# Performance work log

Hardware: AMD Instinct MI355X
Metric: run time of the kernel (lower is better)

The kernel has to match this reference:

```python
import jax, jax.numpy as jnp
import numpy as np
import math

B, N, F = 32, 1024, 64      # batch, nodes, input_dim (data_size)
PRE = 64                     # preweight (== input_dim so output Linear works)
L1 = 128                     # layer_1


def setup_inputs() -> dict:
    key = jax.random.key(0)
    ks = jax.random.split(key, 12)
    def lin(k, out_d, in_d):
        bound = 1.0 / math.sqrt(in_d)
        kw, kb = jax.random.split(k)
        W = jax.random.uniform(kw, (out_d, in_d), jnp.float32, -bound, bound)
        b = jax.random.uniform(kb, (out_d,), jnp.float32, -bound, bound)
        return W, b
    W_pre, b_pre = lin(ks[0], PRE, F)
    W_fc1, b_fc1 = lin(ks[1], L1, PRE)
    W_keys, b_keys = lin(ks[2], 1, L1)
    W_out, b_out = lin(ks[3], 1, F)
    alpha = jax.random.uniform(ks[4], (1,), jnp.float32)
    x = jax.random.normal(ks[5], (B, N, F), jnp.float32)
    adjacency_matrix = jax.random.uniform(ks[6], (B, N, N), jnp.float32)
    return {
        "x": x, "adjacency_matrix": adjacency_matrix, "alpha": alpha,
        "W_pre": W_pre, "b_pre": b_pre, "W_fc1": W_fc1, "b_fc1": b_fc1,
        "W_keys": W_keys, "b_keys": b_keys, "W_out": W_out, "b_out": b_out,
    }


def reference(x, adjacency_matrix, alpha, W_pre, b_pre, W_fc1, b_fc1,
              W_keys, b_keys, W_out, b_out):
    # --- D^-1/2 A D^-1/2 normalization (D is diagonal -> row/col scaling) ---
    deg = adjacency_matrix.sum(axis=-1)                       # [B, N]
    deg = jnp.where(deg != 0, deg, 1.0)
    d_isqrt = deg ** -0.5                                     # [B, N]
    A_norm = d_isqrt[:, :, None] * adjacency_matrix * d_isqrt[:, None, :]
    # --- (alpha*I + A_norm) @ x ---
    h = alpha[0] * x + jnp.einsum('bij,bjf->bif', A_norm, x)  # [B, N, F]
    # --- node embedding (pre_weighting + relu) ---
    values = jax.nn.relu(h @ W_pre.T + b_pre)                 # [B, N, PRE]
    # --- attention pooling (dropout is identity at eval) ---
    queries = jax.nn.relu(values @ W_fc1.T + b_fc1)           # [B, N, L1]
    logits = (queries @ W_keys.T + b_keys)[..., 0]            # [B, N]
    scores = jax.nn.softmax(logits / math.sqrt(2.0), axis=-1) # [B, N]
    vect = jnp.einsum('bn,bnp->bp', scores, values)           # [B, PRE]
    y = vect @ W_out.T + b_out                                # [B, 1]
    return y
```

## Files before the change

kernel.cpp:

```cpp
#include <hip/hip_runtime.h>


#define N_ 1024
#define F_ 64

typedef short s16x8 __attribute__((ext_vector_type(8)));
typedef float f32x4 __attribute__((ext_vector_type(4)));
typedef unsigned short u16x8 __attribute__((ext_vector_type(8)));

__device__ __forceinline__ unsigned short bf16rne(float f) {
  union { float f; unsigned u; } v; v.f = f;
  unsigned r = v.u + 0x7fffu + ((v.u >> 16) & 1u);
  return (unsigned short)(r >> 16);
}

__device__ __forceinline__ void fma_row(float (&a)[4], const float4 av,
                                        const float4 x0, const float4 x1,
                                        const float4 x2, const float4 x3) {
  a[0] += av.x * x0.x + av.y * x1.x + av.z * x2.x + av.w * x3.x;
  a[1] += av.x * x0.y + av.y * x1.y + av.z * x2.y + av.w * x3.y;
  a[2] += av.x * x0.z + av.y * x1.z + av.z * x2.z + av.w * x3.z;
  a[3] += av.x * x0.w + av.y * x1.w + av.z * x2.w + av.w * x3.w;
}

__device__ __forceinline__ void stage16(const void* g, void* l) {
  auto gp = reinterpret_cast<const __attribute__((address_space(1))) void*>(
      reinterpret_cast<uintptr_t>(g));
  auto lp = reinterpret_cast<__attribute__((address_space(3))) void*>(
      reinterpret_cast<uintptr_t>(l));
  __builtin_amdgcn_global_load_lds(gp, lp, 16, 0, 0);
}

__global__ __launch_bounds__(256) void k_deg(const float* __restrict__ A,
                                             float* __restrict__ disq) {
  const int row  = blockIdx.x * 4 + (threadIdx.x >> 6);
  const int lane = threadIdx.x & 63;
  const float4* a4 = (const float4*)(A + (size_t)row * N_);
  float s = 0.f;
#pragma unroll
  for (int it = 0; it < 4; ++it) {
    float4 v = a4[it * 64 + lane];
    s += v.x + v.y + v.z + v.w;
  }
#pragma unroll
  for (int off = 32; off > 0; off >>= 1) s += __shfl_down(s, off, 64);
  if (lane == 0) {
    float d = (s != 0.f) ? s : 1.f;
    disq[row] = rsqrtf(d);
  }
}

__global__ __launch_bounds__(256) void k_xt(const float* __restrict__ x,
                                            const float* __restrict__ disq,
                                            unsigned short* __restrict__ xtb) {
  __shared__ float xs[64][68];
  const int b = blockIdx.y, j0 = blockIdx.x * 64, t = threadIdx.x;
  const float* xb = x + ((size_t)b << 16);
  const float* dq = disq + (b << 10);
#pragma unroll
  for (int it = 0; it < 4; ++it) {
    int idx = it * 1024 + t * 4;
    int jj = idx >> 6, ff = idx & 63;
    float4 vv = *(const float4*)&xb[(size_t)(j0 + jj) * F_ + ff];
    float sc = dq[j0 + jj];
    vv.x *= sc; vv.y *= sc; vv.z *= sc; vv.w *= sc;
    *(float4*)&xs[jj][ff] = vv;
  }
  __syncthreads();
  const int f = t & 63, ch = t >> 6;
  u16x8 o0, o1;
#pragma unroll
  for (int jj = 0; jj < 8; ++jj) o0[jj] = bf16rne(xs[ch * 16 + jj][f]);
#pragma unroll
  for (int jj = 0; jj < 8; ++jj) o1[jj] = bf16rne(xs[ch * 16 + 8 + jj][f]);
  unsigned short* dst = xtb + (size_t)(b * 64 + f) * N_ + j0 + ch * 16;
  *(u16x8*)dst = o0;
  *(u16x8*)(dst + 8) = o1;
}

__global__ __launch_bounds__(256, 3) void k_spmm_mlp(const float* __restrict__ Af,
                                                     const unsigned short* __restrict__ xtb,
                                                     const float* __restrict__ x,
                                                     const float* __restrict__ disq,
                                                     const float* __restrict__ alphap,
                                                     const float* __restrict__ Wpre,
                                                     const float* __restrict__ bpre,
                                                     const float* __restrict__ Wfc1,
                                                     const float* __restrict__ bfc1,
                                                     const float* __restrict__ Wkeys,
                                                     const float* __restrict__ bkeysp,
                                                     float* __restrict__ values,
                                                     float* __restrict__ logits) {
  __shared__ __attribute__((aligned(16))) char smem[54272];
  float (*hs)[68]   = (float(*)[68])(smem);
  float (*wft)[128] = (float(*)[128])(smem + 17408);
  float (*part)[16] = (float(*)[16])(smem + 50176);

  const int t  = threadIdx.x;
  const int b  = blockIdx.x;
  const int i0 = blockIdx.y * 64;
  const int w  = t >> 6, l = t & 63;
  const int lr = l & 15, kq = l >> 4;
  const size_t bb = ((size_t)b << 20);

  const int half = (w & 1) * 32;
  const int srow4 = l >> 4;
  const int mslot = l & 15;
  const float* gA0 = Af + bb + (size_t)(i0 + half + srow4) * 1024;
  int xoff[4];
#pragma unroll
  for (int q = 0; q < 4; ++q) xoff[q] = (mslot ^ ((q * 4 + srow4) & 15)) << 2;
  const int srow8 = l >> 3;
  const int schB  = ((l & 7) ^ srow8) * 8;
  const unsigned short* gsB = xtb + (size_t)(b * 64 + half + srow8) * N_ + schB;

  auto STAGE = [&](char* bufp, int ksv) {
    if (w < 2) {
      const int ko = ksv * 64;
#pragma unroll
      for (int j = 0; j < 8; ++j)
        stage16(gA0 + (size_t)j * 4096 + xoff[j & 3] + ko,
                bufp + (half + j * 4) * 256);
    } else {
      const int ko = ksv * 64;
#pragma unroll
      for (int j = 0; j < 4; ++j)
        stage16(gsB + (size_t)j * 8 * N_ + ko,
                bufp + 16384 + half * 128 + j * 1024);
    }
  };

  STAGE(smem, 0);
  __syncthreads();

  f32x4 acc0 = {0.f, 0.f, 0.f, 0.f}, acc1 = acc0, acc2 = acc0, acc3 = acc0;
  const int arow = w * 16 + lr;
  const int swB = (lr & 7) << 4;
  int cur = 0;

  for (int ks = 0; ks < 16; ++ks) {
    if (ks < 15) STAGE(smem + (cur ^ 1) * 24576, ks + 1);
    const char* cb = smem + cur * 24576;
#pragma unroll
    for (int s = 0; s < 2; ++s) {
      const int m0 = s * 8 + kq * 2;
      f32x4 alo = *(const f32x4*)(cb + arow * 256 + ((m0 ^ lr) << 4));
      f32x4 ahi = *(const f32x4*)(cb + arow * 256 + (((m0 + 1) ^ lr) << 4));
      s16x8 af;
      af[0] = (short)bf16rne(alo[0]); af[1] = (short)bf16rne(alo[1]);
      af[2] = (short)bf16rne(alo[2]); af[3] = (short)bf16rne(alo[3]);
      af[4] = (short)bf16rne(ahi[0]); af[5] = (short)bf16rne(ahi[1]);
      af[6] = (short)bf16rne(ahi[2]); af[7] = (short)bf16rne(ahi[3]);
      const int ch = ((kq + 4 * s) << 4);
      s16x8 b0 = *(const s16x8*)(cb + 16384 + (0 * 16 + lr) * 128 + (ch ^ swB));
      s16x8 b1 = *(const s16x8*)(cb + 16384 + (1 * 16 + lr) * 128 + (ch ^ swB));
      s16x8 b2 = *(const s16x8*)(cb + 16384 + (2 * 16 + lr) * 128 + (ch ^ swB));
      s16x8 b3 = *(const s16x8*)(cb + 16384 + (3 * 16 + lr) * 128 + (ch ^ swB));
      acc0 = __builtin_amdgcn_mfma_f32_16x16x32_bf16(af, b0, acc0, 0, 0, 0);
      acc1 = __builtin_amdgcn_mfma_f32_16x16x32_bf16(af, b1, acc1, 0, 0, 0);
      acc2 = __builtin_amdgcn_mfma_f32_16x16x32_bf16(af, b2, acc2, 0, 0, 0);
      acc3 = __builtin_amdgcn_mfma_f32_16x16x32_bf16(af, b3, acc3, 0, 0, 0);
    }
    __syncthreads();
    cur ^= 1;
  }

  const float alpha = alphap[0];
  const float* dq = disq + (b << 10);
  const float* xb = x + ((size_t)b << 16);
  const int rl = w * 16 + kq * 4;
#pragma unroll
  for (int r = 0; r < 4; ++r) {
    float di = dq[i0 + rl + r];
    size_t ro = (size_t)(i0 + rl + r) * F_;
    hs[rl + r][0  + lr] = alpha * xb[ro + 0  + lr] + di * acc0[r];
    hs[rl + r][16 + lr] = alpha * xb[ro + 16 + lr] + di * acc1[r];
    hs[rl + r][32 + lr] = alpha * xb[ro + 32 + lr] + di * acc2[r];
    hs[rl + r][48 + lr] = alpha * xb[ro + 48 + lr] + di * acc3[r];
  }
#pragma unroll
  for (int it = 0; it < 4; ++it) {
    int idx = it * 1024 + t * 4;
    float4 wv = *(const float4*)&Wpre[idx];
    int p = idx >> 6, f = idx & 63;
    wft[f + 0][p] = wv.x; wft[f + 1][p] = wv.y; wft[f + 2][p] = wv.z; wft[f + 3][p] = wv.w;
  }
  __syncthreads();

  const size_t base = ((size_t)(b * 16 + blockIdx.y)) * 4096;
  const int cg = t & 15, rg = t >> 4;
  float acc[4][4] = {{0.f}};
#pragma unroll
  for (int q = 0; q < 16; ++q) {
    float4 xv0 = *(float4*)&wft[q * 4 + 0][cg * 4];
    float4 xv1 = *(float4*)&wft[q * 4 + 1][cg * 4];
    float4 xv2 = *(float4*)&wft[q * 4 + 2][cg * 4];
    float4 xv3 = *(float4*)&wft[q * 4 + 3][cg * 4];
#pragma unroll
    for (int k = 0; k < 4; ++k) {
      float4 av = *(float4*)&hs[rg * 4 + k][q * 4];
      fma_row(acc[k], av, xv0, xv1, xv2, xv3);
    }
  }
  float4 bp = *(const float4*)&bpre[cg * 4];
  __syncthreads();
#pragma unroll
  for (int k = 0; k < 4; ++k) {
    float4 o;
    o.x = fmaxf(acc[k][0] + bp.x, 0.f);
    o.y = fmaxf(acc[k][1] + bp.y, 0.f);
    o.z = fmaxf(acc[k][2] + bp.z, 0.f);
    o.w = fmaxf(acc[k][3] + bp.w, 0.f);
    *(float4*)&hs[rg * 4 + k][cg * 4] = o;
    *(float4*)&values[base + (size_t)(rg * 4 + k) * 64 + cg * 4] = o;
  }
#pragma unroll
  for (int it = 0; it < 8; ++it) {
    int idx = it * 1024 + t * 4;
    int ll = idx >> 6, p = idx & 63;
    float4 wv = *(const float4*)&Wfc1[idx];
    wft[p + 0][ll] = wv.x; wft[p + 1][ll] = wv.y; wft[p + 2][ll] = wv.z; wft[p + 3][ll] = wv.w;
  }
  __syncthreads();

  const int lg = cg;
  float acc_a[4][4] = {{0.f}};
  float acc_b[4][4] = {{0.f}};
#pragma unroll
  for (int q = 0; q < 16; ++q) {
    float4 w0a = *(float4*)&wft[q * 4 + 0][lg * 8];
    float4 w0b = *(float4*)&wft[q * 4 + 0][lg * 8 + 4];
    float4 w1a = *(float4*)&wft[q * 4 + 1][lg * 8];
    float4 w1b = *(float4*)&wft[q * 4 + 1][lg * 8 + 4];
    float4 w2a = *(float4*)&wft[q * 4 + 2][lg * 8];
    float4 w2b = *(float4*)&wft[q * 4 + 2][lg * 8 + 4];
    float4 w3a = *(float4*)&wft[q * 4 + 3][lg * 8];
    float4 w3b = *(float4*)&wft[q * 4 + 3][lg * 8 + 4];
#pragma unroll
    for (int k = 0; k < 4; ++k) {
      float4 vv = *(float4*)&hs[rg * 4 + k][q * 4];
      fma_row(acc_a[k], vv, w0a, w1a, w2a, w3a);
      fma_row(acc_b[k], vv, w0b, w1b, w2b, w3b);
    }
  }
  float4 bfa = *(const float4*)&bfc1[lg * 8];
  float4 bfb = *(const float4*)&bfc1[lg * 8 + 4];
  float4 wka = *(const float4*)&Wkeys[lg * 8];
  float4 wkb = *(const float4*)&Wkeys[lg * 8 + 4];
#pragma unroll
  for (int k = 0; k < 4; ++k) {
    float lp = 0.f;
    lp += fmaxf(acc_a[k][0] + bfa.x, 0.f) * wka.x;
    lp += fmaxf(acc_a[k][1] + bfa.y, 0.f) * wka.y;
    lp += fmaxf(acc_a[k][2] + bfa.z, 0.f) * wka.z;
    lp += fmaxf(acc_a[k][3] + bfa.w, 0.f) * wka.w;
    lp += fmaxf(acc_b[k][0] + bfb.x, 0.f) * wkb.x;
    lp += fmaxf(acc_b[k][1] + bfb.y, 0.f) * wkb.y;
    lp += fmaxf(acc_b[k][2] + bfb.z, 0.f) * wkb.z;
    lp += fmaxf(acc_b[k][3] + bfb.w, 0.f) * wkb.w;
    part[rg * 4 + k][lg] = lp;
  }
  __syncthreads();
  if (t < 64) {
    float s = bkeysp[0];
#pragma unroll
    for (int g = 0; g < 16; ++g) s += part[t][g];
    logits[(b * 16 + blockIdx.y) * 64 + t] = s;
  }
}

__global__ __launch_bounds__(1024) void k_tail(const float* __restrict__ logits,
                                               const float* __restrict__ values,
                                               float* __restrict__ vpart) {
  const int c = blockIdx.x, b = blockIdx.y, t = threadIdx.x;
  __shared__ float sc[1024];
  __shared__ float red[16];
  __shared__ float pool[16][64];
  const float isq2 = 0.70710678118654752f;
  float lv = logits[(b << 10) + t] * isq2;
  float m = lv;
#pragma unroll
  for (int off = 32; off > 0; off >>= 1) m = fmaxf(m, __shfl_xor(m, off, 64));
  if ((t & 63) == 0) red[t >> 6] = m;
  __syncthreads();
  m = red[0];
#pragma unroll
  for (int i = 1; i < 16; ++i) m = fmaxf(m, red[i]);
  float e = expf(lv - m);
  float s = e;
#pragma unroll
  for (int off = 32; off > 0; off >>= 1) s += __shfl_xor(s, off, 64);
  __syncthreads();
  if ((t & 63) == 0) red[t >> 6] = s;
  __syncthreads();
  s = red[0];
#pragma unroll
  for (int i = 1; i < 16; ++i) s += red[i];
  sc[t] = e * (1.f / s);
  __syncthreads();
  const int col = t & 63, g = t >> 6;
  const float* vb = values + ((size_t)b << 16);
  float acc = 0.f;
#pragma unroll
  for (int k = 0; k < 8; ++k) {
    int n = c * 128 + g + 16 * k;
    acc += sc[n] * vb[(size_t)n * 64 + col];
  }
  pool[g][col] = acc;
  __syncthreads();
  if (t < 64) {
    float v = 0.f;
#pragma unroll
    for (int gg = 0; gg < 16; ++gg) v += pool[gg][t];
    vpart[(b * 8 + c) * 64 + t] = v;
  }
}

__global__ __launch_bounds__(256) void k_out(const float* __restrict__ vpart,
                                             const float* __restrict__ Wout,
                                             const float* __restrict__ boutp,
                                             float* __restrict__ y) {
  const int t = threadIdx.x, w = t >> 6, lane = t & 63;
#pragma unroll
  for (int it = 0; it < 8; ++it) {
    int b = w * 8 + it;
    float v = 0.f;
#pragma unroll
    for (int ch = 0; ch < 8; ++ch) v += vpart[(b * 8 + ch) * 64 + lane];
    float p = v * Wout[lane];
#pragma unroll
    for (int off = 32; off > 0; off >>= 1) p += __shfl_down(p, off, 64);
    if (lane == 0) y[b] = p + boutp[0];
  }
}

extern "C" void kernel_launch(void* const* d_in, const int* in_sizes, int n_in,
                              void* d_out, int out_size, void* d_ws, size_t ws_size,
                              hipStream_t stream) {
  const float* x     = (const float*)d_in[0];
  const float* A     = (const float*)d_in[1];
  const float* alpha = (const float*)d_in[2];
  const float* Wpre  = (const float*)d_in[3];
  const float* bpre  = (const float*)d_in[4];
  const float* Wfc1  = (const float*)d_in[5];
  const float* bfc1  = (const float*)d_in[6];
  const float* Wkeys = (const float*)d_in[7];
  const float* bkeys = (const float*)d_in[8];
  const float* Wout  = (const float*)d_in[9];
  const float* bout  = (const float*)d_in[10];
  float* y = (float*)d_out;

  float* ws     = (float*)d_ws;
  float* disq   = ws;
  float* values = disq + 32768;
  float* logits = values + 2097152;
  float* vpart  = logits + 32768;
  unsigned short* xtb = (unsigned short*)(vpart + 16384);

  k_deg     <<<dim3(8192),   dim3(256),  0, stream>>>(A, disq);
  k_xt      <<<dim3(16, 32), dim3(256),  0, stream>>>(x, disq, xtb);
  k_spmm_mlp<<<dim3(32, 16), dim3(256),  0, stream>>>(A, xtb, x, disq, alpha,
                                                      Wpre, bpre, Wfc1, bfc1, Wkeys, bkeys,
                                                      values, logits);
  k_tail    <<<dim3(8, 32),  dim3(1024), 0, stream>>>(logits, values, vpart);
  k_out     <<<dim3(1),      dim3(256),  0, stream>>>(vpart, Wout, bout, y);
}
```

Before: 76.88 us.

## Fuse degree and x-transpose kernels; fold output reduction into tail via counter

Merges the degree computation and the scaled bf16 transpose of x into one kernel, so each block computes the degrees for its 16 rows and uses them right away instead of reading them back from global memory in a second launch. The final output reduction is folded into the tail kernel using an atomic counter, where the last block to finish computes y. This removes two kernel launches and their inter-kernel gaps. In exchange it adds threadfences, an atomic, and a counter reset that relies on launch ordering.

```diff
diff --git a/kernel.cpp b/kernel.cpp
--- a/kernel.cpp
+++ b/kernel.cpp
@@ -6,7 +6,7 @@
 
 typedef short s16x8 __attribute__((ext_vector_type(8)));
 typedef float f32x4 __attribute__((ext_vector_type(4)));
-typedef unsigned short u16x8 __attribute__((ext_vector_type(8)));
+typedef unsigned short u16x4 __attribute__((ext_vector_type(4)));
 
 __device__ __forceinline__ unsigned short bf16rne(float f) {
   union { float f; unsigned u; } v; v.f = f;
@@ -31,51 +31,49 @@
   __builtin_amdgcn_global_load_lds(gp, lp, 16, 0, 0);
 }
 
-__global__ __launch_bounds__(256) void k_deg(const float* __restrict__ A,
-                                             float* __restrict__ disq) {
-  const int row  = blockIdx.x * 4 + (threadIdx.x >> 6);
-  const int lane = threadIdx.x & 63;
-  const float4* a4 = (const float4*)(A + (size_t)row * N_);
-  float s = 0.f;
-#pragma unroll
-  for (int it = 0; it < 4; ++it) {
-    float4 v = a4[it * 64 + lane];
-    s += v.x + v.y + v.z + v.w;
-  }
-#pragma unroll
-  for (int off = 32; off > 0; off >>= 1) s += __shfl_down(s, off, 64);
-  if (lane == 0) {
-    float d = (s != 0.f) ? s : 1.f;
-    disq[row] = rsqrtf(d);
-  }
-}
-
-__global__ __launch_bounds__(256) void k_xt(const float* __restrict__ x,
-                                            const float* __restrict__ disq,
-                                            unsigned short* __restrict__ xtb) {
-  __shared__ float xs[64][68];
-  const int b = blockIdx.y, j0 = blockIdx.x * 64, t = threadIdx.x;
-  const float* xb = x + ((size_t)b << 16);
-  const float* dq = disq + (b << 10);
-#pragma unroll
-  for (int it = 0; it < 4; ++it) {
-    int idx = it * 1024 + t * 4;
-    int jj = idx >> 6, ff = idx & 63;
-    float4 vv = *(const float4*)&xb[(size_t)(j0 + jj) * F_ + ff];
-    float sc = dq[j0 + jj];
-    vv.x *= sc; vv.y *= sc; vv.z *= sc; vv.w *= sc;
-    *(float4*)&xs[jj][ff] = vv;
-  }
-  __syncthreads();
-  const int f = t & 63, ch = t >> 6;
-  u16x8 o0, o1;
-#pragma unroll
-  for (int jj = 0; jj < 8; ++jj) o0[jj] = bf16rne(xs[ch * 16 + jj][f]);
-#pragma unroll
-  for (int jj = 0; jj < 8; ++jj) o1[jj] = bf16rne(xs[ch * 16 + 8 + jj][f]);
-  unsigned short* dst = xtb + (size_t)(b * 64 + f) * N_ + j0 + ch * 16;
-  *(u16x8*)dst = o0;
-  *(u16x8*)(dst + 8) = o1;
+__global__ __launch_bounds__(256) void k_degxt(const float* __restrict__ A,
+                                               const float* __restrict__ x,
+                                               float* __restrict__ disq,
+                                               unsigned short* __restrict__ xtb,
+                                               int* __restrict__ counter) {
+  __shared__ float xs[16][68];
+  __shared__ float dsq[16];
+  const int jt = blockIdx.x, b = blockIdx.y;
+  const int j0 = jt * 16;
+  const int t = threadIdx.x, w = t >> 6, l = t & 63;
+  if (jt == 0 && b == 0 && t == 0) *counter = 0;
+
+  const float* Ab = A + ((size_t)b << 20) + (size_t)j0 * N_;
+#pragma unroll
+  for (int i = 0; i < 4; ++i) {
+    const int r = w * 4 + i;
+    const float4* rp = (const float4*)(Ab + (size_t)r * N_);
+    float s = 0.f;
+#pragma unroll
+    for (int c = 0; c < 4; ++c) {
+      float4 v = rp[c * 64 + l];
+      s += v.x + v.y + v.z + v.w;
+    }
+#pragma unroll
+    for (int off = 32; off > 0; off >>= 1) s += __shfl_down(s, off, 64);
+    if (l == 0) {
+      float d = (s != 0.f) ? s : 1.f;
+      float di = rsqrtf(d);
+      dsq[r] = di;
+      disq[(b << 10) + j0 + r] = di;
+    }
+  }
+  {
+    int idx = t * 4, jj = idx >> 6, ff = idx & 63;
+    *(float4*)&xs[jj][ff] =
+        *(const float4*)&x[((size_t)b << 16) + (size_t)(j0 + jj) * F_ + ff];
+  }
+  __syncthreads();
+  const int f = l, js = w * 4;
+  u16x4 o4;
+#pragma unroll
+  for (int jj = 0; jj < 4; ++jj) o4[jj] = bf16rne(xs[js + jj][f] * dsq[js + jj]);
+  *(u16x4*)(xtb + (size_t)(b * 64 + f) * N_ + j0 + js) = o4;
 }
 
 __global__ __launch_bounds__(256, 3) void k_spmm_mlp(const float* __restrict__ Af,
@@ -269,13 +267,18 @@
   }
 }
 
-__global__ __launch_bounds__(1024) void k_tail(const float* __restrict__ logits,
-                                               const float* __restrict__ values,
-                                               float* __restrict__ vpart) {
+__global__ __launch_bounds__(1024) void k_tailout(const float* __restrict__ logits,
+                                                  const float* __restrict__ values,
+                                                  const float* __restrict__ Wout,
+                                                  const float* __restrict__ boutp,
+                                                  float* __restrict__ vpart,
+                                                  int* __restrict__ counter,
+                                                  float* __restrict__ y) {
   const int c = blockIdx.x, b = blockIdx.y, t = threadIdx.x;
   __shared__ float sc[1024];
   __shared__ float red[16];
   __shared__ float pool[16][64];
+  __shared__ int is_last;
   const float isq2 = 0.70710678118654752f;
   float lv = logits[(b << 10) + t] * isq2;
   float m = lv;
@@ -314,23 +317,23 @@
     for (int gg = 0; gg < 16; ++gg) v += pool[gg][t];
     vpart[(b * 8 + c) * 64 + t] = v;
   }
-}
-
-__global__ __launch_bounds__(256) void k_out(const float* __restrict__ vpart,
-                                             const float* __restrict__ Wout,
-                                             const float* __restrict__ boutp,
-                                             float* __restrict__ y) {
-  const int t = threadIdx.x, w = t >> 6, lane = t & 63;
-#pragma unroll
-  for (int it = 0; it < 8; ++it) {
-    int b = w * 8 + it;
-    float v = 0.f;
-#pragma unroll
-    for (int ch = 0; ch < 8; ++ch) v += vpart[(b * 8 + ch) * 64 + lane];
-    float p = v * Wout[lane];
-#pragma unroll
-    for (int off = 32; off > 0; off >>= 1) p += __shfl_down(p, off, 64);
-    if (lane == 0) y[b] = p + boutp[0];
+  __threadfence();
+  if (t == 0) is_last = (atomicAdd(counter, 1) == 255);
+  __syncthreads();
+  if (is_last) {
+    __threadfence();
+    const int wv = t >> 6, l = t & 63;
+#pragma unroll
+    for (int rep = 0; rep < 2; ++rep) {
+      int bo = wv * 2 + rep;
+      float v = 0.f;
+#pragma unroll
+      for (int ch = 0; ch < 8; ++ch) v += vpart[(bo * 8 + ch) * 64 + l];
+      float p = v * Wout[l];
+#pragma unroll
+      for (int off = 32; off > 0; off >>= 1) p += __shfl_down(p, off, 64);
+      if (l == 0) y[bo] = p + boutp[0];
+    }
   }
 }
 
@@ -356,12 +359,12 @@
   float* logits = values + 2097152;
   float* vpart  = logits + 32768;
   unsigned short* xtb = (unsigned short*)(vpart + 16384);
-
-  k_deg     <<<dim3(8192),   dim3(256),  0, stream>>>(A, disq);
-  k_xt      <<<dim3(16, 32), dim3(256),  0, stream>>>(x, disq, xtb);
+  int* counter = (int*)(xtb + 2097152);
+
+  k_degxt   <<<dim3(64, 32), dim3(256),  0, stream>>>(A, x, disq, xtb, counter);
   k_spmm_mlp<<<dim3(32, 16), dim3(256),  0, stream>>>(A, xtb, x, disq, alpha,
                                                       Wpre, bpre, Wfc1, bfc1, Wkeys, bkeys,
                                                       values, logits);
-  k_tail    <<<dim3(8, 32),  dim3(1024), 0, stream>>>(logits, values, vpart);
-  k_out     <<<dim3(1),      dim3(256),  0, stream>>>(vpart, Wout, bout, y);
-}
+  k_tailout <<<dim3(8, 32),  dim3(1024), 0, stream>>>(logits, values, Wout, bout,
+                                                      vpart, counter, y);
+}
```

New measurement: 135.7 us. 76.5% more time.
